# Kernel tuning notes

Measured on AMD Instinct MI355X. Metric: run time of the kernel, lower is better.

Reference implementation:

```python
import jax, jax.numpy as jnp
import numpy as np
from jax import lax

B, T = 128, 1024
RNN_DIM, EMB_DIM, ATT_DIM = 1024, 512, 128
N_FILT, KSIZE = 32, 31
PAD = KSIZE // 2  # 15


def setup_inputs() -> dict:
    key = jax.random.key(0)
    ks = jax.random.split(key, 8)
    return {
        "attention_hidden_state": jax.random.normal(ks[0], (B, RNN_DIM), jnp.float32),
        "memory": jax.random.normal(ks[1], (B, T, EMB_DIM), jnp.float32),
        "processed_memory": jax.random.normal(ks[2], (B, T, ATT_DIM), jnp.float32),
        "attention_weights_cat": jax.random.uniform(ks[3], (B, 2, T), jnp.float32),
        "mask": jnp.zeros((B, T), dtype=bool),
        # learned params
        "w_query": jax.random.normal(ks[4], (RNN_DIM, ATT_DIM), jnp.float32) * 0.02,
        "w_conv": jax.random.normal(ks[5], (N_FILT, 2, KSIZE), jnp.float32) * 0.1,   # OIH
        "w_loc": jax.random.normal(ks[6], (N_FILT, ATT_DIM), jnp.float32) * 0.1,
        "v": jax.random.normal(ks[7], (ATT_DIM,), jnp.float32) * 0.1,
    }


def reference(attention_hidden_state, memory, processed_memory,
              attention_weights_cat, mask, w_query, w_conv, w_loc, v):
    # processed_query: [B, 1, A] (broadcast over T)
    pq = (attention_hidden_state @ w_query)[:, None, :]
    # location features: Conv1d(2 -> N_FILT, pad=K//2, no bias) then Linear(N_FILT -> A)
    conv = lax.conv_general_dilated(
        attention_weights_cat, w_conv, window_strides=(1,),
        padding=[(PAD, PAD)], dimension_numbers=("NCH", "OIH", "NCH"))  # [B, F, T]
    loc = jnp.einsum("bft,fa->bta", conv, w_loc)  # [B, T, A]
    # energies: v^T tanh(pq + loc + pmem)  -> [B, T]
    energies = jnp.tanh(pq + loc + processed_memory) @ v
    energies = jnp.where(mask, -jnp.inf, energies)
    attention_weights = jax.nn.softmax(energies, axis=1)  # [B, T]
    attention_context = jnp.einsum("bt,btd->bd", attention_weights, memory)
    return attention_context, attention_weights
```

## Files before the change

kernel.cpp:

```cpp
#include <hip/hip_runtime.h>
#include <math.h>

#define BB    128
#define TT    1024
#define RNN   1024
#define EMBD  512
#define ATTD  128
#define NFILT 32
#define KSZ   31
#define PADK  15
#define CK    62
#define SPLIT 16
#define TSP   (TT / SPLIT)

__device__ __forceinline__ float fast_tanhf(float x) {
  const float ax = fabsf(x);
  const float t  = __expf(-2.f * ax);
  const float r  = (1.f - t) / (1.f + t);
  return copysignf(r, x);
}

__global__ __launch_bounds__(256) void k_pq_wl(const float* __restrict__ hid,
                                               const float* __restrict__ wq,
                                               const float* __restrict__ wconv,
                                               const float* __restrict__ wloc,
                                               float* __restrict__ pq,
                                               float* __restrict__ wl) {
  const int tid = threadIdx.x;
  if (blockIdx.x < BB) {
    const int b  = blockIdx.x;
    const int a  = tid & (ATTD - 1);
    const int kh = tid >> 7;
    __shared__ float sh[RNN];
    __shared__ float sred[ATTD];
    for (int i = tid; i < RNN; i += 256) sh[i] = hid[(size_t)b * RNN + i];
    __syncthreads();
    float acc = 0.f;
    const int k0 = kh * (RNN / 2);
    #pragma unroll 8
    for (int k = 0; k < RNN / 2; ++k)
      acc = fmaf(sh[k0 + k], wq[(size_t)(k0 + k) * ATTD + a], acc);
    if (kh == 1) sred[a] = acc;
    __syncthreads();
    if (kh == 0) pq[(size_t)b * ATTD + a] = acc + sred[a];
  } else {
    const int idx = (blockIdx.x - BB) * 256 + tid;
    const int ck = idx >> 7;
    const int a  = idx & (ATTD - 1);
    float acc = 0.f;
    #pragma unroll
    for (int f = 0; f < NFILT; ++f)
      acc = fmaf(wconv[f * CK + ck], wloc[f * ATTD + a], acc);
    wl[idx] = acc;
  }
}

__global__ __launch_bounds__(128, 3) void k_fused(
    const float* __restrict__ awc,
    const float* __restrict__ pmem,
    const float* __restrict__ mem,
    const float* __restrict__ wl,
    const float* __restrict__ vvec,
    const float* __restrict__ pq,
    const unsigned char* __restrict__ mask,
    float* __restrict__ wts,
    float* __restrict__ part_ctx,
    float* __restrict__ part_ms,
    float* __restrict__ part_sum)
{
  const int blk  = blockIdx.x;
  const int b    = blk & (BB - 1);
  const int s    = blk >> 7;
  const int tid  = threadIdx.x;
  const int lane = tid & 63;
  const int wave = tid >> 6;
  const int t0   = s * TSP;

  __shared__ float s_aw[2][TSP + 30];
  __shared__ float s_p[TSP];

  for (int i = tid; i < 2 * (TSP + 30); i += 128) {
    const int c  = (i >= TSP + 30);
    const int j  = c ? i - (TSP + 30) : i;
    const int tg = t0 - PADK + j;
    s_aw[c][j] = (tg >= 0 && tg < TT) ? awc[((size_t)b * 2 + c) * TT + tg] : 0.f;
  }

  float2 wlr[CK];
  const float2* wl2 = (const float2*)wl;
  #pragma unroll
  for (int ck = 0; ck < CK; ++ck) wlr[ck] = wl2[ck * 64 + lane];
  const float2 pq2 = ((const float2*)(pq + (size_t)b * ATTD))[lane];
  const float2 v2  = ((const float2*)vvec)[lane];
  const float2* pm2 = (const float2*)(pmem + (size_t)b * TT * ATTD);
  __syncthreads();

  for (int i = 0; i < TSP / 2; ++i) {
    const int tl = wave * (TSP / 2) + i;
    const int tg = t0 + tl;
    const float2 pm = pm2[(size_t)tg * 64 + lane];
    float x0 = pq2.x + pm.x;
    float x1 = pq2.y + pm.y;
    #pragma unroll
    for (int k = 0; k < KSZ; ++k) {
      const float a0 = s_aw[0][tl + k];
      x0 = fmaf(a0, wlr[k].x, x0);
      x1 = fmaf(a0, wlr[k].y, x1);
    }
    #pragma unroll
    for (int k = 0; k < KSZ; ++k) {
      const float a1 = s_aw[1][tl + k];
      x0 = fmaf(a1, wlr[KSZ + k].x, x0);
      x1 = fmaf(a1, wlr[KSZ + k].y, x1);
    }
    float e = v2.x * fast_tanhf(x0) + v2.y * fast_tanhf(x1);
    #pragma unroll
    for (int off = 32; off; off >>= 1) e += __shfl_xor(e, off);
    if (lane == 0) s_p[tl] = e;
  }
  __syncthreads();

  if (wave == 0) {
    float e = s_p[lane];
    if (mask[(size_t)b * TT + t0 + lane]) e = -INFINITY;
    float m = e;
    #pragma unroll
    for (int off = 32; off; off >>= 1) m = fmaxf(m, __shfl_xor(m, off));
    const float p = __expf(e - m);
    float sum = p;
    #pragma unroll
    for (int off = 32; off; off >>= 1) sum += __shfl_xor(sum, off);
    s_p[lane] = p;
    wts[(size_t)b * TT + t0 + lane] = p;
    if (lane == 0) {
      part_ms [(size_t)s * BB + b] = m;
      part_sum[(size_t)s * BB + b] = sum;
    }
  }
  __syncthreads();

  const float4* m4 = (const float4*)(mem + (size_t)b * TT * EMBD) + (size_t)t0 * (EMBD / 4);
  float4 acc = make_float4(0.f, 0.f, 0.f, 0.f);
  #pragma unroll 8
  for (int t = 0; t < TSP; ++t) {
    const float p  = s_p[t];
    const float4 mv = m4[(size_t)t * (EMBD / 4) + tid];
    acc.x = fmaf(p, mv.x, acc.x);
    acc.y = fmaf(p, mv.y, acc.y);
    acc.z = fmaf(p, mv.z, acc.z);
    acc.w = fmaf(p, mv.w, acc.w);
  }
  ((float4*)part_ctx)[((size_t)s * BB + b) * (EMBD / 4) + tid] = acc;
}

__global__ __launch_bounds__(128) void k_combine(
    const float* __restrict__ part_ctx,
    const float* __restrict__ part_ms,
    const float* __restrict__ part_sum,
    float* __restrict__ ctx,
    float* __restrict__ wts)
{
  const int b   = blockIdx.x;
  const int tid = threadIdx.x;
  __shared__ float s_a[SPLIT];

  float M = -INFINITY;
  #pragma unroll
  for (int s = 0; s < SPLIT; ++s) M = fmaxf(M, part_ms[(size_t)s * BB + b]);
  float T = 0.f;
  #pragma unroll
  for (int s = 0; s < SPLIT; ++s)
    T += part_sum[(size_t)s * BB + b] * __expf(part_ms[(size_t)s * BB + b] - M);
  const float invT = 1.f / T;
  if (tid < SPLIT) s_a[tid] = __expf(part_ms[(size_t)tid * BB + b] - M) * invT;
  __syncthreads();

  float4 acc = make_float4(0.f, 0.f, 0.f, 0.f);
  #pragma unroll
  for (int s = 0; s < SPLIT; ++s) {
    const float a = s_a[s];
    const float4 v = ((const float4*)part_ctx)[((size_t)s * BB + b) * (EMBD / 4) + tid];
    acc.x = fmaf(a, v.x, acc.x);
    acc.y = fmaf(a, v.y, acc.y);
    acc.z = fmaf(a, v.z, acc.z);
    acc.w = fmaf(a, v.w, acc.w);
  }
  ((float4*)ctx)[(size_t)b * (EMBD / 4) + tid] = acc;

  #pragma unroll
  for (int i = 0; i < TT / 128; ++i) {
    const int t = i * 128 + tid;
    wts[(size_t)b * TT + t] *= s_a[t >> 6];
  }
}

extern "C" void kernel_launch(void* const* d_in, const int* in_sizes, int n_in,
                              void* d_out, int out_size, void* d_ws, size_t ws_size,
                              hipStream_t stream) {
  const float* hid   = (const float*)d_in[0];
  const float* mem   = (const float*)d_in[1];
  const float* pmem  = (const float*)d_in[2];
  const float* awc   = (const float*)d_in[3];
  const unsigned char* mask = (const unsigned char*)d_in[4];
  const float* wq    = (const float*)d_in[5];
  const float* wconv = (const float*)d_in[6];
  const float* wloc  = (const float*)d_in[7];
  const float* v     = (const float*)d_in[8];

  float* out = (float*)d_out;
  float* ctx = out;
  float* wts = out + BB * EMBD;

  char* ws = (char*)d_ws;
  float* pq       = (float*)(ws);
  float* wl       = (float*)(ws + (64 << 10));
  float* part_ms  = (float*)(ws + (128 << 10));
  float* part_sum = (float*)(ws + (192 << 10));
  float* part_ctx = (float*)(ws + (1 << 20));

  k_pq_wl<<<BB + 31, 256, 0, stream>>>(hid, wq, wconv, wloc, pq, wl);
  k_fused<<<SPLIT * BB, 128, 0, stream>>>(awc, pmem, mem, wl, v, pq, mask,
                                          wts, part_ctx, part_ms, part_sum);
  k_combine<<<BB, 128, 0, stream>>>(part_ctx, part_ms, part_sum, ctx, wts);
}
```

Baseline: 498.7 us.

## Split attention dims across waves, double T-split, and prefetch processed memory

The fused kernel now splits the sequence into twice as many chunks and runs 256 threads per block. Each lane handles one attention dimension instead of two, with wave pairs covering the two halves of the attention dimension and combining energies through shared memory. The next processed-memory row is software-prefetched, and the context accumulation uses float2 across 256 threads. This raises parallelism and occupancy and halves the per-thread register footprint of the location weights, at the cost of more partial contexts to combine and an extra shared-memory reduction step.

```diff
diff --git a/kernel.cpp b/kernel.cpp
--- a/kernel.cpp
+++ b/kernel.cpp
@@ -10,7 +10,7 @@
 #define KSZ   31
 #define PADK  15
 #define CK    62
-#define SPLIT 16
+#define SPLIT 32
 #define TSP   (TT / SPLIT)
 
 __device__ __forceinline__ float fast_tanhf(float x) {
@@ -55,7 +55,7 @@
   }
 }
 
-__global__ __launch_bounds__(128, 3) void k_fused(
+__global__ __launch_bounds__(256, 4) void k_fused(
     const float* __restrict__ awc,
     const float* __restrict__ pmem,
     const float* __restrict__ mem,
@@ -77,61 +77,62 @@
   const int t0   = s * TSP;
 
   __shared__ float s_aw[2][TSP + 30];
+  __shared__ float s_e[TSP][2];
   __shared__ float s_p[TSP];
 
-  for (int i = tid; i < 2 * (TSP + 30); i += 128) {
+  for (int i = tid; i < 2 * (TSP + 30); i += 256) {
     const int c  = (i >= TSP + 30);
     const int j  = c ? i - (TSP + 30) : i;
     const int tg = t0 - PADK + j;
     s_aw[c][j] = (tg >= 0 && tg < TT) ? awc[((size_t)b * 2 + c) * TT + tg] : 0.f;
   }
 
-  float2 wlr[CK];
-  const float2* wl2 = (const float2*)wl;
-  #pragma unroll
-  for (int ck = 0; ck < CK; ++ck) wlr[ck] = wl2[ck * 64 + lane];
-  const float2 pq2 = ((const float2*)(pq + (size_t)b * ATTD))[lane];
-  const float2 v2  = ((const float2*)vvec)[lane];
-  const float2* pm2 = (const float2*)(pmem + (size_t)b * TT * ATTD);
-  __syncthreads();
-
+  const int a = ((wave & 1) << 6) + lane;
+  float wlr[CK];
+  #pragma unroll
+  for (int ck = 0; ck < CK; ++ck) wlr[ck] = wl[ck * ATTD + a];
+  const float pqv = pq[(size_t)b * ATTD + a];
+  const float vv  = vvec[a];
+  const float* pmb = pmem + (size_t)b * TT * ATTD;
+  __syncthreads();
+
+  const int tg0 = (wave >> 1) * (TSP / 2);
+  float pm_next = pmb[(size_t)(t0 + tg0) * ATTD + a];
   for (int i = 0; i < TSP / 2; ++i) {
-    const int tl = wave * (TSP / 2) + i;
-    const int tg = t0 + tl;
-    const float2 pm = pm2[(size_t)tg * 64 + lane];
-    float x0 = pq2.x + pm.x;
-    float x1 = pq2.y + pm.y;
+    const int tl = tg0 + i;
+    const float pm = pm_next;
+    if (i + 1 < TSP / 2) pm_next = pmb[(size_t)(t0 + tl + 1) * ATTD + a];
+    float x0 = pqv + pm;
+    float x1 = 0.f;
     #pragma unroll
     for (int k = 0; k < KSZ; ++k) {
-      const float a0 = s_aw[0][tl + k];
-      x0 = fmaf(a0, wlr[k].x, x0);
-      x1 = fmaf(a0, wlr[k].y, x1);
-    }
-    #pragma unroll
-    for (int k = 0; k < KSZ; ++k) {
-      const float a1 = s_aw[1][tl + k];
-      x0 = fmaf(a1, wlr[KSZ + k].x, x0);
-      x1 = fmaf(a1, wlr[KSZ + k].y, x1);
-    }
-    float e = v2.x * fast_tanhf(x0) + v2.y * fast_tanhf(x1);
-    #pragma unroll
-    for (int off = 32; off; off >>= 1) e += __shfl_xor(e, off);
-    if (lane == 0) s_p[tl] = e;
+      x0 = fmaf(s_aw[0][tl + k], wlr[k], x0);
+      x1 = fmaf(s_aw[1][tl + k], wlr[KSZ + k], x1);
+    }
+    float pe = vv * fast_tanhf(x0 + x1);
+    #pragma unroll
+    for (int off = 32; off; off >>= 1) pe += __shfl_xor(pe, off);
+    if (lane == 0) s_e[tl][wave & 1] = pe;
   }
   __syncthreads();
 
   if (wave == 0) {
-    float e = s_p[lane];
-    if (mask[(size_t)b * TT + t0 + lane]) e = -INFINITY;
+    float e = -INFINITY;
+    if (lane < TSP) {
+      e = s_e[lane][0] + s_e[lane][1];
+      if (mask[(size_t)b * TT + t0 + lane]) e = -INFINITY;
+    }
     float m = e;
     #pragma unroll
     for (int off = 32; off; off >>= 1) m = fmaxf(m, __shfl_xor(m, off));
-    const float p = __expf(e - m);
+    const float p = (lane < TSP) ? __expf(e - m) : 0.f;
     float sum = p;
     #pragma unroll
     for (int off = 32; off; off >>= 1) sum += __shfl_xor(sum, off);
-    s_p[lane] = p;
-    wts[(size_t)b * TT + t0 + lane] = p;
+    if (lane < TSP) {
+      s_p[lane] = p;
+      wts[(size_t)b * TT + t0 + lane] = p;
+    }
     if (lane == 0) {
       part_ms [(size_t)s * BB + b] = m;
       part_sum[(size_t)s * BB + b] = sum;
@@ -139,18 +140,16 @@
   }
   __syncthreads();
 
-  const float4* m4 = (const float4*)(mem + (size_t)b * TT * EMBD) + (size_t)t0 * (EMBD / 4);
-  float4 acc = make_float4(0.f, 0.f, 0.f, 0.f);
+  const float2* m2 = (const float2*)(mem + ((size_t)b * TT + t0) * EMBD);
+  float2 acc = make_float2(0.f, 0.f);
   #pragma unroll 8
   for (int t = 0; t < TSP; ++t) {
-    const float p  = s_p[t];
-    const float4 mv = m4[(size_t)t * (EMBD / 4) + tid];
+    const float p   = s_p[t];
+    const float2 mv = m2[(size_t)t * (EMBD / 2) + tid];
     acc.x = fmaf(p, mv.x, acc.x);
     acc.y = fmaf(p, mv.y, acc.y);
-    acc.z = fmaf(p, mv.z, acc.z);
-    acc.w = fmaf(p, mv.w, acc.w);
-  }
-  ((float4*)part_ctx)[((size_t)s * BB + b) * (EMBD / 4) + tid] = acc;
+  }
+  ((float2*)part_ctx)[((size_t)s * BB + b) * (EMBD / 2) + tid] = acc;
 }
 
 __global__ __launch_bounds__(128) void k_combine(
@@ -190,7 +189,7 @@
   #pragma unroll
   for (int i = 0; i < TT / 128; ++i) {
     const int t = i * 128 + tid;
-    wts[(size_t)b * TT + t] *= s_a[t >> 6];
+    wts[(size_t)b * TT + t] *= s_a[t / TSP];
   }
 }
 
@@ -215,11 +214,11 @@
   float* pq       = (float*)(ws);
   float* wl       = (float*)(ws + (64 << 10));
   float* part_ms  = (float*)(ws + (128 << 10));
-  float* part_sum = (float*)(ws + (192 << 10));
+  float* part_sum = (float*)(ws + (256 << 10));
   float* part_ctx = (float*)(ws + (1 << 20));
 
   k_pq_wl<<<BB + 31, 256, 0, stream>>>(hid, wq, wconv, wloc, pq, wl);
-  k_fused<<<SPLIT * BB, 128, 0, stream>>>(awc, pmem, mem, wl, v, pq, mask,
+  k_fused<<<SPLIT * BB, 256, 0, stream>>>(awc, pmem, mem, wl, v, pq, mask,
                                           wts, part_ctx, part_ms, part_sum);
   k_combine<<<BB, 128, 0, stream>>>(part_ctx, part_ms, part_sum, ctx, wts);
 }
```

After: 470.3 us. 5.7% less time.
